# Optimization experiments

Measured on AMD Instinct MI355X. Metric: run time of the kernel, lower is better.

The kernel has to match this reference:

```python
import jax, jax.numpy as jnp
import numpy as np

WS = 8   # window_size
SS = 4   # shift_size
NH = 12  # num_heads
DIM = 384
HD = DIM // NH


def _rel_index():
    coords = np.stack(np.meshgrid(np.arange(WS), np.arange(WS), indexing='ij'))  # (2, ws, ws)
    cf = coords.reshape(2, -1)                       # (2, n)
    rel = (cf[:, :, None] - cf[:, None, :]).transpose(1, 2, 0).copy()  # (n, n, 2)
    rel[..., 0] += WS - 1
    rel[..., 1] += WS - 1
    rel[..., 0] *= 2 * WS - 1
    return rel.sum(-1)                               # (n, n) int


def _attn_mask(h, w):
    img = np.zeros((h, w))
    sl = (slice(0, -WS), slice(-WS, -SS), slice(-SS, None))
    cnt = 0
    for hs in sl:
        for ws_ in sl:
            img[hs, ws_] = cnt
            cnt += 1
    mw = img.reshape(h // WS, WS, w // WS, WS).transpose(0, 2, 1, 3).reshape(-1, WS * WS)  # (nW, n)
    d = mw[:, None, :] - mw[:, :, None]
    return np.where(d != 0, -100.0, 0.0).astype(np.float32)  # (nW, n, n)


def setup_inputs() -> dict:
    key = jax.random.key(0)
    ks = jax.random.split(key, 10)
    B, H, W = 32, 64, 64
    std = 0.02
    return {
        'x': jax.random.normal(ks[0], (B, H, W, DIM), jnp.float32),
        'wq': jax.random.normal(ks[1], (DIM, DIM), jnp.float32) * std,
        'bq': jnp.zeros((DIM,), jnp.float32),
        'wk': jax.random.normal(ks[2], (DIM, DIM), jnp.float32) * std,
        'bk': jnp.zeros((DIM,), jnp.float32),
        'wv': jax.random.normal(ks[3], (DIM, DIM), jnp.float32) * std,
        'bv': jnp.zeros((DIM,), jnp.float32),
        'wo': jax.random.normal(ks[4], (DIM, DIM), jnp.float32) * std,
        'bo': jnp.zeros((DIM,), jnp.float32),
        'bias_table': jax.random.normal(ks[5], ((2 * WS - 1) ** 2, NH), jnp.float32) * std,
    }


def reference(x, wq, bq, wk, bk, wv, bv, wo, bo, bias_table):
    b, h, w, c = x.shape
    pad_h = (-h) % WS
    pad_w = (-w) % WS
    if pad_h or pad_w:
        x = jnp.pad(x, ((0, 0), (0, pad_h), (0, pad_w), (0, 0)))
    hp, wp = x.shape[1], x.shape[2]

    if SS > 0:
        x_sh = jnp.roll(x, shift=(-SS, -SS), axis=(1, 2))
        mask = jnp.asarray(_attn_mask(hp, wp))          # (nW, n, n)
    else:
        x_sh = x
        mask = None

    # window partition -> (B*nW, n, C)
    nwh, nww = hp // WS, wp // WS
    win = x_sh.reshape(b, nwh, WS, nww, WS, c).transpose(0, 1, 3, 2, 4, 5)
    win = win.reshape(-1, WS * WS, c)
    b_, n, _ = win.shape

    scale = HD ** -0.5
    q = (win @ wq.T + bq).reshape(b_, n, NH, HD).transpose(0, 2, 1, 3) * scale
    k = (win @ wk.T + bk).reshape(b_, n, NH, HD).transpose(0, 2, 1, 3)
    v = (win @ wv.T + bv).reshape(b_, n, NH, HD).transpose(0, 2, 1, 3)

    attn = jnp.einsum('bhnd,bhmd->bhnm', q, k)          # (b_, NH, n, n)
    rel = bias_table[jnp.asarray(_rel_index()).reshape(-1)].reshape(n, n, NH)
    attn = attn + rel.transpose(2, 0, 1)[None]
    if mask is not None:
        nW = mask.shape[0]
        attn = attn.reshape(b_ // nW, nW, NH, n, n) + mask[None, :, None]
        attn = attn.reshape(b_, NH, n, n)
    attn = jax.nn.softmax(attn, axis=-1)

    out = jnp.einsum('bhnm,bhmd->bhnd', attn, v).transpose(0, 2, 1, 3).reshape(b_, n, c)
    out = out @ wo.T + bo

    # window reverse -> (B, hp, wp, C)
    out = out.reshape(b, nwh, nww, WS, WS, c).transpose(0, 1, 3, 2, 4, 5).reshape(b, hp, wp, c)
    if SS > 0:
        out = jnp.roll(out, shift=(SS, SS), axis=(1, 2))
    return out[:, :h, :w, :]
```

## Files before the change

### kernel.cpp

```cpp
#include <hip/hip_runtime.h>
#include <hip/hip_bf16.h>

typedef short bf16x8 __attribute__((ext_vector_type(8)));
typedef float f32x4 __attribute__((ext_vector_type(4)));

#define NH_ 12
#define DIM_ 384

static __device__ __forceinline__ float bf2f_us(ushort u) {
    __hip_bfloat16 h; __builtin_memcpy(&h, &u, 2);
    return __bfloat162float(h);
}
static __device__ __forceinline__ ushort f2us(float f) {
    __hip_bfloat16 h = __float2bfloat16(f);
    ushort u; __builtin_memcpy(&u, &h, 2);
    return u;
}

static __device__ __forceinline__ void gload_lds16(const void* g, void* l) {
    __builtin_amdgcn_global_load_lds(
        (const __attribute__((address_space(1))) unsigned int*)g,
        (__attribute__((address_space(3))) unsigned int*)l, 16, 0, 0);
}

static __device__ __forceinline__ int regioncnt(int t, int wr, int wc) {
    int rr = (wr == 7) ? (((t >> 3) < 4) ? 1 : 2) : 0;
    int cc = (wc == 7) ? (((t & 7) < 4) ? 1 : 2) : 0;
    return rr * 3 + cc;
}

__global__ __launch_bounds__(256) void convert_kernel(
    const float* wq, const float* wk, const float* wv, const float* wo,
    const float* bq, const float* bk, const float* bv, const float* bo,
    const float* bt, ushort* __restrict__ dst)
{
    const int N = 594060;
    for (int i = blockIdx.x * 256 + threadIdx.x; i < N; i += gridDim.x * 256) {
        const float* src; int off;
        if (i < 589824) {
            int wsel = i / 147456; off = i - wsel * 147456;
            src = (wsel == 0) ? wq : (wsel == 1) ? wk : (wsel == 2) ? wv : wo;
        } else if (i < 591360) {
            int bsel = (i - 589824) / 384; off = (i - 589824) - bsel * 384;
            src = (bsel == 0) ? bq : (bsel == 1) ? bk : (bsel == 2) ? bv : bo;
        } else {
            off = i - 591360; src = bt;
        }
        dst[i] = f2us(src[off]);
    }
}

__global__ void bias_kernel(const ushort* __restrict__ tablec, float* __restrict__ biasmat) {
    int i = blockIdx.x;
    int j = threadIdx.x;
    int idx = ((i >> 3) - (j >> 3) + 7) * 15 + ((i & 7) - (j & 7) + 7);
    #pragma unroll
    for (int h = 0; h < NH_; ++h)
        biasmat[h * 4096 + i * 64 + j] = bf2f_us(tablec[idx * NH_ + h]);
}

__global__ __launch_bounds__(256, 4) void qkv_gemm(
    const float* __restrict__ x, const ushort* __restrict__ wb,
    ushort* __restrict__ qws, ushort* __restrict__ kws, ushort* __restrict__ vws,
    int wbase, int nmb)
{
    __shared__ __align__(16) ushort As[2][4096];
    __shared__ __align__(16) ushort Bs[2][4096];
    const int nwg = nmb * 9;
    const int orig = blockIdx.x;
    const int wgid = (orig & 7) * (nwg >> 3) + (orig >> 3);
    const int mb = wgid / 9, nt = wgid - mb * 9;
    const int wsel = nt / 3, ntm = nt - wsel * 3;
    const int n0 = nt * 128;
    const int tid = threadIdx.x, lane = tid & 63, wv = tid >> 6;
    const int col16 = lane & 15, quad = lane >> 4;
    const int wm = wv >> 1, wn = wv & 1;

    const int kof = ((tid >> 1) & 3) * 8 + (tid & 1) * 4;
    const float* arow[4];
    #pragma unroll
    for (int it = 0; it < 4; ++it) {
        const int s = it * 128 + (tid >> 1);
        const int row = (s >> 6) * 16 + ((s & 63) >> 2);
        const int wglob = wbase + mb * 2 + (row >> 6);
        const int token = row & 63;
        const int b = wglob >> 6, widx = wglob & 63, wr = widx >> 3, wc = widx & 7;
        const int orr = (wr * 8 + (token >> 3) + 4) & 63;
        const int occ = (wc * 8 + (token & 7) + 4) & 63;
        arow[it] = x + (((size_t)b * 64 + orr) * 64 + occ) * DIM_ + kof;
    }

    const ushort* bsrc = wb + (size_t)n0 * DIM_;
    const int brow_l = lane >> 2, bkof = (lane & 3) * 8;

    f32x4 acc[4][4];
    #pragma unroll
    for (int i2 = 0; i2 < 4; ++i2)
        #pragma unroll
        for (int j2 = 0; j2 < 4; ++j2)
            acc[i2][j2] = (f32x4){0.f, 0.f, 0.f, 0.f};

    const int NK = DIM_ / 32;

    #pragma unroll
    for (int c2 = 0; c2 < 2; ++c2) {
        const int blk = wv * 2 + c2;
        gload_lds16(bsrc + (size_t)(blk * 16 + brow_l) * DIM_ + bkof, &Bs[0][blk * 512]);
    }
    #pragma unroll
    for (int it = 0; it < 4; ++it) {
        const float4 v = *reinterpret_cast<const float4*>(arow[it]);
        ushort4 u4; u4.x = f2us(v.x); u4.y = f2us(v.y); u4.z = f2us(v.z); u4.w = f2us(v.w);
        *reinterpret_cast<ushort4*>(&As[0][it * 1024 + tid * 4]) = u4;
    }
    __syncthreads();

    for (int t = 0; t < NK; ++t) {
        const int cur = t & 1, nxt = cur ^ 1;
        const int kk = t * 32;
        float4 av[4];
        if (t + 1 < NK) {
            #pragma unroll
            for (int it = 0; it < 4; ++it)
                av[it] = *reinterpret_cast<const float4*>(arow[it] + kk + 32);
            #pragma unroll
            for (int c2 = 0; c2 < 2; ++c2) {
                const int blk = wv * 2 + c2;
                gload_lds16(bsrc + (size_t)(blk * 16 + brow_l) * DIM_ + kk + 32 + bkof,
                            &Bs[nxt][blk * 512]);
            }
        }
        bf16x8 af[4], bfm[4];
        #pragma unroll
        for (int rt = 0; rt < 4; ++rt)
            af[rt] = *reinterpret_cast<const bf16x8*>(
                &As[cur][(wm * 4 + rt) * 512 + (col16 * 4 + quad) * 8]);
        #pragma unroll
        for (int ct = 0; ct < 4; ++ct)
            bfm[ct] = *reinterpret_cast<const bf16x8*>(
                &Bs[cur][(wn * 4 + ct) * 512 + (col16 * 4 + quad) * 8]);
        #pragma unroll
        for (int rt = 0; rt < 4; ++rt)
            #pragma unroll
            for (int ct = 0; ct < 4; ++ct)
                acc[rt][ct] = __builtin_amdgcn_mfma_f32_16x16x32_bf16(af[rt], bfm[ct], acc[rt][ct], 0, 0, 0);
        if (t + 1 < NK) {
            #pragma unroll
            for (int it = 0; it < 4; ++it) {
                ushort4 u4;
                u4.x = f2us(av[it].x); u4.y = f2us(av[it].y);
                u4.z = f2us(av[it].z); u4.w = f2us(av[it].w);
                *reinterpret_cast<ushort4*>(&As[nxt][it * 1024 + tid * 4]) = u4;
            }
        }
        __syncthreads();
    }

    const int lw = mb * 2 + wm;
    const float scale = 0.17677669529663687f;
    const ushort* bias_all = wb + 589824 + wsel * 384;
    #pragma unroll
    for (int ct = 0; ct < 4; ++ct) {
        const int jl = ntm * 128 + wn * 64 + ct * 16 + col16;
        const int head = jl >> 5, hd = jl & 31;
        const float bj = bf2f_us(bias_all[jl]);
        #pragma unroll
        for (int rt = 0; rt < 4; ++rt) {
            if (wsel == 2) {
                ushort4 pk;
                pk.x = f2us(acc[rt][ct][0] + bj);
                pk.y = f2us(acc[rt][ct][1] + bj);
                pk.z = f2us(acc[rt][ct][2] + bj);
                pk.w = f2us(acc[rt][ct][3] + bj);
                *reinterpret_cast<ushort4*>(
                    vws + ((size_t)(lw * NH_ + head) * 32 + hd) * 64 + rt * 16 + quad * 4) = pk;
            } else {
                #pragma unroll
                for (int r = 0; r < 4; ++r) {
                    const int token = rt * 16 + quad * 4 + r;
                    const float v = acc[rt][ct][r] + bj;
                    if (wsel == 0)
                        qws[((size_t)(lw * NH_ + head) * 64 + token) * 32 + hd] = f2us(v * scale);
                    else
                        kws[((size_t)(lw * NH_ + head) * 64 + token) * 32 + hd] = f2us(v);
                }
            }
        }
    }
}

__global__ __launch_bounds__(64) void attn_kernel(
    const __hip_bfloat16* __restrict__ qws, const __hip_bfloat16* __restrict__ kws,
    const __hip_bfloat16* __restrict__ vws, const float* __restrict__ biasmat,
    __hip_bfloat16* __restrict__ attnout, int wbase)
{
    __shared__ __align__(16) __hip_bfloat16 Pbuf[64 * 72];
    const int bid = blockIdx.x;
    const int lw = bid / NH_, h = bid - lw * NH_;
    const int w = wbase + lw;
    const int lane = threadIdx.x, col16 = lane & 15, quad = lane >> 4;
    const ushort* qp = reinterpret_cast<const ushort*>(qws) + ((size_t)lw * NH_ + h) * 64 * 32;
    const ushort* kp = reinterpret_cast<const ushort*>(kws) + ((size_t)lw * NH_ + h) * 64 * 32;
    const ushort* vp = reinterpret_cast<const ushort*>(vws) + ((size_t)lw * NH_ + h) * 32 * 64;

    bf16x8 aq[4], bk4[4];
    #pragma unroll
    for (int t = 0; t < 4; ++t) {
        aq[t]  = *reinterpret_cast<const bf16x8*>(qp + (t * 16 + col16) * 32 + quad * 8);
        bk4[t] = *reinterpret_cast<const bf16x8*>(kp + (t * 16 + col16) * 32 + quad * 8);
    }
    f32x4 S[4][4];
    #pragma unroll
    for (int rt = 0; rt < 4; ++rt) {
        #pragma unroll
        for (int ct = 0; ct < 4; ++ct) {
            f32x4 z = {0.f,0.f,0.f,0.f};
            S[rt][ct] = __builtin_amdgcn_mfma_f32_16x16x32_bf16(aq[rt], bk4[ct], z, 0, 0, 0);
        }
    }

    const int widx = w & 63, wr = widx >> 3, wc = widx & 7;
    #pragma unroll
    for (int ct = 0; ct < 4; ++ct) {
        const int jj = ct * 16 + col16;
        const int cntj = regioncnt(jj, wr, wc);
        #pragma unroll
        for (int rt = 0; rt < 4; ++rt) {
            #pragma unroll
            for (int r = 0; r < 4; ++r) {
                const int ii = rt * 16 + quad * 4 + r;
                float add = biasmat[h * 4096 + ii * 64 + jj];
                if (regioncnt(ii, wr, wc) != cntj) add -= 100.f;
                S[rt][ct][r] += add;
            }
        }
    }

    #pragma unroll
    for (int rt = 0; rt < 4; ++rt) {
        float rm[4], rs[4];
        #pragma unroll
        for (int r = 0; r < 4; ++r)
            rm[r] = fmaxf(fmaxf(S[rt][0][r], S[rt][1][r]), fmaxf(S[rt][2][r], S[rt][3][r]));
        #pragma unroll
        for (int d = 1; d <= 8; d <<= 1) {
            #pragma unroll
            for (int r = 0; r < 4; ++r) rm[r] = fmaxf(rm[r], __shfl_xor(rm[r], d, 64));
        }
        #pragma unroll
        for (int r = 0; r < 4; ++r) rs[r] = 0.f;
        #pragma unroll
        for (int ct = 0; ct < 4; ++ct) {
            #pragma unroll
            for (int r = 0; r < 4; ++r) {
                float p = __expf(S[rt][ct][r] - rm[r]);
                S[rt][ct][r] = p;
                rs[r] += p;
            }
        }
        #pragma unroll
        for (int d = 1; d <= 8; d <<= 1) {
            #pragma unroll
            for (int r = 0; r < 4; ++r) rs[r] += __shfl_xor(rs[r], d, 64);
        }
        #pragma unroll
        for (int ct = 0; ct < 4; ++ct) {
            #pragma unroll
            for (int r = 0; r < 4; ++r) {
                const float inv = 1.0f / rs[r];
                Pbuf[(rt * 16 + quad * 4 + r) * 72 + ct * 16 + col16] =
                    __float2bfloat16(S[rt][ct][r] * inv);
            }
        }
    }
    __syncthreads();

    f32x4 O[4][2];
    #pragma unroll
    for (int rt = 0; rt < 4; ++rt) {
        f32x4 z = {0.f,0.f,0.f,0.f};
        O[rt][0] = z; O[rt][1] = z;
    }
    const ushort* pb = reinterpret_cast<const ushort*>(Pbuf);
    #pragma unroll
    for (int ks = 0; ks < 2; ++ks) {
        bf16x8 bv0 = *reinterpret_cast<const bf16x8*>(vp + (col16)*64 + ks * 32 + quad * 8);
        bf16x8 bv1 = *reinterpret_cast<const bf16x8*>(vp + (16 + col16) * 64 + ks * 32 + quad * 8);
        #pragma unroll
        for (int rt = 0; rt < 4; ++rt) {
            bf16x8 ap = *reinterpret_cast<const bf16x8*>(pb + (rt * 16 + col16) * 72 + ks * 32 + quad * 8);
            O[rt][0] = __builtin_amdgcn_mfma_f32_16x16x32_bf16(ap, bv0, O[rt][0], 0, 0, 0);
            O[rt][1] = __builtin_amdgcn_mfma_f32_16x16x32_bf16(ap, bv1, O[rt][1], 0, 0, 0);
        }
    }
    __hip_bfloat16* op = attnout + (size_t)lw * 64 * DIM_ + h * 32;
    #pragma unroll
    for (int rt = 0; rt < 4; ++rt) {
        #pragma unroll
        for (int c2 = 0; c2 < 2; ++c2) {
            #pragma unroll
            for (int r = 0; r < 4; ++r) {
                const int token = rt * 16 + quad * 4 + r;
                op[token * DIM_ + c2 * 16 + col16] = __float2bfloat16(O[rt][c2][r]);
            }
        }
    }
}

__global__ __launch_bounds__(256, 4) void proj_gemm(
    const ushort* __restrict__ attnin, const ushort* __restrict__ wb,
    float* __restrict__ out, int wbase, int nmb)
{
    __shared__ __align__(16) ushort As[2][4096];
    __shared__ __align__(16) ushort Bs[2][4096];
    const int nwg = nmb * 3;
    const int orig = blockIdx.x;
    const int wgid = (orig & 7) * (nwg >> 3) + (orig >> 3);
    const int mb = wgid / 3, nt = wgid - mb * 3;
    const int n0 = nt * 128;
    const int tid = threadIdx.x, lane = tid & 63, wv = tid >> 6;
    const int col16 = lane & 15, quad = lane >> 4;
    const int wm = wv >> 1, wn = wv & 1;

    const ushort* asrc = attnin + (size_t)mb * 128 * DIM_;
    const ushort* bsrc = wb + (size_t)3 * 147456 + (size_t)n0 * DIM_;
    const int row_l = lane >> 2, kof_l = (lane & 3) * 8;

    f32x4 acc[4][4];
    #pragma unroll
    for (int i2 = 0; i2 < 4; ++i2)
        #pragma unroll
        for (int j2 = 0; j2 < 4; ++j2)
            acc[i2][j2] = (f32x4){0.f, 0.f, 0.f, 0.f};

    const int NK = DIM_ / 32;

    #pragma unroll
    for (int c2 = 0; c2 < 2; ++c2) {
        const int blk = wv * 2 + c2;
        gload_lds16(asrc + (size_t)(blk * 16 + row_l) * DIM_ + kof_l, &As[0][blk * 512]);
        gload_lds16(bsrc + (size_t)(blk * 16 + row_l) * DIM_ + kof_l, &Bs[0][blk * 512]);
    }
    __syncthreads();

    for (int t = 0; t < NK; ++t) {
        const int cur = t & 1, nxt = cur ^ 1;
        const int kk = t * 32;
        if (t + 1 < NK) {
            #pragma unroll
            for (int c2 = 0; c2 < 2; ++c2) {
                const int blk = wv * 2 + c2;
                gload_lds16(asrc + (size_t)(blk * 16 + row_l) * DIM_ + kk + 32 + kof_l,
                            &As[nxt][blk * 512]);
                gload_lds16(bsrc + (size_t)(blk * 16 + row_l) * DIM_ + kk + 32 + kof_l,
                            &Bs[nxt][blk * 512]);
            }
        }
        bf16x8 af[4], bfm[4];
        #pragma unroll
        for (int rt = 0; rt < 4; ++rt)
            af[rt] = *reinterpret_cast<const bf16x8*>(
                &As[cur][(wm * 4 + rt) * 512 + (col16 * 4 + quad) * 8]);
        #pragma unroll
        for (int ct = 0; ct < 4; ++ct)
            bfm[ct] = *reinterpret_cast<const bf16x8*>(
                &Bs[cur][(wn * 4 + ct) * 512 + (col16 * 4 + quad) * 8]);
        #pragma unroll
        for (int rt = 0; rt < 4; ++rt)
            #pragma unroll
            for (int ct = 0; ct < 4; ++ct)
                acc[rt][ct] = __builtin_amdgcn_mfma_f32_16x16x32_bf16(af[rt], bfm[ct], acc[rt][ct], 0, 0, 0);
        __syncthreads();
    }

    const int lw = mb * 2 + wm;
    const int wglob = wbase + lw;
    const int b = wglob >> 6, widx = wglob & 63, wr = widx >> 3, wc = widx & 7;
    const ushort* boc = wb + 589824 + 3 * 384;
    #pragma unroll
    for (int ct = 0; ct < 4; ++ct) {
        const int j = n0 + wn * 64 + ct * 16 + col16;
        const float bj = bf2f_us(boc[j]);
        #pragma unroll
        for (int rt = 0; rt < 4; ++rt) {
            #pragma unroll
            for (int r = 0; r < 4; ++r) {
                const int token = rt * 16 + quad * 4 + r;
                const int orr = (wr * 8 + (token >> 3) + 4) & 63;
                const int occ = (wc * 8 + (token & 7) + 4) & 63;
                out[(((size_t)b * 64 + orr) * 64 + occ) * DIM_ + j] = acc[rt][ct][r] + bj;
            }
        }
    }
}

extern "C" void kernel_launch(void* const* d_in, const int* in_sizes, int n_in,
                              void* d_out, int out_size, void* d_ws, size_t ws_size,
                              hipStream_t stream) {
    const float* x = (const float*)d_in[0];
    float* out = (float*)d_out;
    char* ws = (char*)d_ws;

    ushort* wb      = (ushort*)ws;
    float*  biasmat = (float*)(ws + 1188352);
    const size_t FIXED = 1384960;

    int wchunk = 128;
    const int cands[4] = {2048, 1024, 512, 256};
    for (int i = 0; i < 4; ++i) {
        if (FIXED + (size_t)cands[i] * 4 * 49152 <= ws_size) { wchunk = cands[i]; break; }
    }
    const size_t CQ = (size_t)wchunk * NH_ * 64 * 32 * 2;
    __hip_bfloat16* qws = (__hip_bfloat16*)(ws + FIXED);
    __hip_bfloat16* kws = (__hip_bfloat16*)(ws + FIXED + CQ);
    __hip_bfloat16* vws = (__hip_bfloat16*)(ws + FIXED + 2 * CQ);
    __hip_bfloat16* att = (__hip_bfloat16*)(ws + FIXED + 3 * CQ);

    convert_kernel<<<dim3(512), dim3(256), 0, stream>>>(
        (const float*)d_in[1], (const float*)d_in[3], (const float*)d_in[5], (const float*)d_in[7],
        (const float*)d_in[2], (const float*)d_in[4], (const float*)d_in[6], (const float*)d_in[8],
        (const float*)d_in[9], wb);
    bias_kernel<<<dim3(64), dim3(64), 0, stream>>>(wb + 591360, biasmat);

    for (int c = 0; c < 2048 / wchunk; ++c) {
        const int wbase = c * wchunk;
        const int nmb = wchunk / 2;
        qkv_gemm<<<dim3(nmb * 9), dim3(256), 0, stream>>>(
            x, wb, (ushort*)qws, (ushort*)kws, (ushort*)vws, wbase, nmb);
        attn_kernel<<<dim3(wchunk * NH_), dim3(64), 0, stream>>>(qws, kws, vws, biasmat, att, wbase);
        proj_gemm<<<dim3(nmb * 3), dim3(256), 0, stream>>>(
            (const ushort*)att, wb, out, wbase, nmb);
    }
}
```

Measured before the change: 777.6 us.

## Precompute bias+mask in fragment layout, pack 4 heads per attention block, change LDS layout

The bias kernel now builds four window-type variants (interior, last row, last column, corner) of relative-position bias plus shift mask, stored in the MFMA accumulator fragment order, so the attention kernel does coalesced float4 loads instead of scattered scalar loads and per-element region tests. The attention kernel runs four heads per 256-thread block, each wave with its own P buffer, which removes the block-wide barrier. The GEMM kernels also change the LDS tile layout so each lane reads a contiguous 16-byte chunk at lane*8, which aims to cut bank conflicts. The cost is a larger precomputed bias buffer and more LDS per attention block.

```diff
diff --git a/kernel.cpp b/kernel.cpp
--- a/kernel.cpp
+++ b/kernel.cpp
@@ -50,13 +50,32 @@
     }
 }
 
-__global__ void bias_kernel(const ushort* __restrict__ tablec, float* __restrict__ biasmat) {
-    int i = blockIdx.x;
-    int j = threadIdx.x;
-    int idx = ((i >> 3) - (j >> 3) + 7) * 15 + ((i & 7) - (j & 7) + 7);
-    #pragma unroll
-    for (int h = 0; h < NH_; ++h)
-        biasmat[h * 4096 + i * 64 + j] = bf2f_us(tablec[idx * NH_ + h]);
+__global__ __launch_bounds__(256) void bias_kernel(
+    const ushort* __restrict__ tablec, float* __restrict__ biasv)
+{
+    const int vh = blockIdx.x;
+    const int v = vh / NH_, h = vh - v * NH_;
+    const int wr = (v & 2) ? 7 : 0, wc = (v & 1) ? 7 : 0;
+    const int tid = threadIdx.x, lane = tid & 63;
+    #pragma unroll
+    for (int i = 0; i < 4; ++i) {
+        const int tno = (tid >> 6) + 4 * i;
+        const int rt = tno >> 2, ct = tno & 3;
+        const int jj = ct * 16 + (lane & 15);
+        const int cntj = regioncnt(jj, wr, wc);
+        float4 o;
+        float vals[4];
+        #pragma unroll
+        for (int r = 0; r < 4; ++r) {
+            const int ii = rt * 16 + (lane >> 4) * 4 + r;
+            const int idx = ((ii >> 3) - (jj >> 3) + 7) * 15 + ((ii & 7) - (jj & 7) + 7);
+            float val = bf2f_us(tablec[idx * NH_ + h]);
+            if (regioncnt(ii, wr, wc) != cntj) val -= 100.f;
+            vals[r] = val;
+        }
+        o.x = vals[0]; o.y = vals[1]; o.z = vals[2]; o.w = vals[3];
+        reinterpret_cast<float4*>(biasv)[((size_t)vh * 16 + tno) * 64 + lane] = o;
+    }
 }
 
 __global__ __launch_bounds__(256, 4) void qkv_gemm(
@@ -76,22 +95,21 @@
     const int col16 = lane & 15, quad = lane >> 4;
     const int wm = wv >> 1, wn = wv & 1;
 
-    const int kof = ((tid >> 1) & 3) * 8 + (tid & 1) * 4;
+    const int kofA = ((tid >> 5) & 3) * 8 + (tid & 1) * 4;
     const float* arow[4];
     #pragma unroll
     for (int it = 0; it < 4; ++it) {
-        const int s = it * 128 + (tid >> 1);
-        const int row = (s >> 6) * 16 + ((s & 63) >> 2);
+        const int row = (it * 2 + (tid >> 7)) * 16 + ((tid >> 1) & 15);
         const int wglob = wbase + mb * 2 + (row >> 6);
         const int token = row & 63;
         const int b = wglob >> 6, widx = wglob & 63, wr = widx >> 3, wc = widx & 7;
         const int orr = (wr * 8 + (token >> 3) + 4) & 63;
         const int occ = (wc * 8 + (token & 7) + 4) & 63;
-        arow[it] = x + (((size_t)b * 64 + orr) * 64 + occ) * DIM_ + kof;
+        arow[it] = x + (((size_t)b * 64 + orr) * 64 + occ) * DIM_ + kofA;
     }
 
     const ushort* bsrc = wb + (size_t)n0 * DIM_;
-    const int brow_l = lane >> 2, bkof = (lane & 3) * 8;
+    const int brow_l = lane & 15, bkof = (lane >> 4) * 8;
 
     f32x4 acc[4][4];
     #pragma unroll
@@ -133,12 +151,10 @@
         bf16x8 af[4], bfm[4];
         #pragma unroll
         for (int rt = 0; rt < 4; ++rt)
-            af[rt] = *reinterpret_cast<const bf16x8*>(
-                &As[cur][(wm * 4 + rt) * 512 + (col16 * 4 + quad) * 8]);
+            af[rt] = *reinterpret_cast<const bf16x8*>(&As[cur][(wm * 4 + rt) * 512 + lane * 8]);
         #pragma unroll
         for (int ct = 0; ct < 4; ++ct)
-            bfm[ct] = *reinterpret_cast<const bf16x8*>(
-                &Bs[cur][(wn * 4 + ct) * 512 + (col16 * 4 + quad) * 8]);
+            bfm[ct] = *reinterpret_cast<const bf16x8*>(&Bs[cur][(wn * 4 + ct) * 512 + lane * 8]);
         #pragma unroll
         for (int rt = 0; rt < 4; ++rt)
             #pragma unroll
@@ -189,16 +205,18 @@
     }
 }
 
-__global__ __launch_bounds__(64) void attn_kernel(
+__global__ __launch_bounds__(256) void attn_kernel(
     const __hip_bfloat16* __restrict__ qws, const __hip_bfloat16* __restrict__ kws,
-    const __hip_bfloat16* __restrict__ vws, const float* __restrict__ biasmat,
+    const __hip_bfloat16* __restrict__ vws, const float* __restrict__ biasv,
     __hip_bfloat16* __restrict__ attnout, int wbase)
 {
-    __shared__ __align__(16) __hip_bfloat16 Pbuf[64 * 72];
+    __shared__ __align__(16) ushort Pbuf[4][64 * 72];
     const int bid = blockIdx.x;
-    const int lw = bid / NH_, h = bid - lw * NH_;
+    const int lw = bid / 3, hg = bid - lw * 3;
+    const int tid = threadIdx.x, wvi = tid >> 6, lane = tid & 63;
+    const int h = hg * 4 + wvi;
     const int w = wbase + lw;
-    const int lane = threadIdx.x, col16 = lane & 15, quad = lane >> 4;
+    const int col16 = lane & 15, quad = lane >> 4;
     const ushort* qp = reinterpret_cast<const ushort*>(qws) + ((size_t)lw * NH_ + h) * 64 * 32;
     const ushort* kp = reinterpret_cast<const ushort*>(kws) + ((size_t)lw * NH_ + h) * 64 * 32;
     const ushort* vp = reinterpret_cast<const ushort*>(vws) + ((size_t)lw * NH_ + h) * 32 * 64;
@@ -220,22 +238,20 @@
     }
 
     const int widx = w & 63, wr = widx >> 3, wc = widx & 7;
-    #pragma unroll
-    for (int ct = 0; ct < 4; ++ct) {
-        const int jj = ct * 16 + col16;
-        const int cntj = regioncnt(jj, wr, wc);
-        #pragma unroll
-        for (int rt = 0; rt < 4; ++rt) {
-            #pragma unroll
-            for (int r = 0; r < 4; ++r) {
-                const int ii = rt * 16 + quad * 4 + r;
-                float add = biasmat[h * 4096 + ii * 64 + jj];
-                if (regioncnt(ii, wr, wc) != cntj) add -= 100.f;
-                S[rt][ct][r] += add;
-            }
-        }
-    }
-
+    const int v = ((wr == 7) ? 2 : 0) + ((wc == 7) ? 1 : 0);
+    const float4* bp = reinterpret_cast<const float4*>(biasv) +
+                       ((size_t)(v * NH_ + h) * 16) * 64 + lane;
+    #pragma unroll
+    for (int rt = 0; rt < 4; ++rt) {
+        #pragma unroll
+        for (int ct = 0; ct < 4; ++ct) {
+            const float4 bb = bp[(rt * 4 + ct) * 64];
+            S[rt][ct][0] += bb.x; S[rt][ct][1] += bb.y;
+            S[rt][ct][2] += bb.z; S[rt][ct][3] += bb.w;
+        }
+    }
+
+    ushort* pb_w = &Pbuf[wvi][0];
     #pragma unroll
     for (int rt = 0; rt < 4; ++rt) {
         float rm[4], rs[4];
@@ -268,12 +284,11 @@
             #pragma unroll
             for (int r = 0; r < 4; ++r) {
                 const float inv = 1.0f / rs[r];
-                Pbuf[(rt * 16 + quad * 4 + r) * 72 + ct * 16 + col16] =
-                    __float2bfloat16(S[rt][ct][r] * inv);
-            }
-        }
-    }
-    __syncthreads();
+                pb_w[(rt * 16 + quad * 4 + r) * 72 + ct * 16 + col16] =
+                    f2us(S[rt][ct][r] * inv);
+            }
+        }
+    }
 
     f32x4 O[4][2];
     #pragma unroll
@@ -281,14 +296,13 @@
         f32x4 z = {0.f,0.f,0.f,0.f};
         O[rt][0] = z; O[rt][1] = z;
     }
-    const ushort* pb = reinterpret_cast<const ushort*>(Pbuf);
     #pragma unroll
     for (int ks = 0; ks < 2; ++ks) {
         bf16x8 bv0 = *reinterpret_cast<const bf16x8*>(vp + (col16)*64 + ks * 32 + quad * 8);
         bf16x8 bv1 = *reinterpret_cast<const bf16x8*>(vp + (16 + col16) * 64 + ks * 32 + quad * 8);
         #pragma unroll
         for (int rt = 0; rt < 4; ++rt) {
-            bf16x8 ap = *reinterpret_cast<const bf16x8*>(pb + (rt * 16 + col16) * 72 + ks * 32 + quad * 8);
+            bf16x8 ap = *reinterpret_cast<const bf16x8*>(pb_w + (rt * 16 + col16) * 72 + ks * 32 + quad * 8);
             O[rt][0] = __builtin_amdgcn_mfma_f32_16x16x32_bf16(ap, bv0, O[rt][0], 0, 0, 0);
             O[rt][1] = __builtin_amdgcn_mfma_f32_16x16x32_bf16(ap, bv1, O[rt][1], 0, 0, 0);
         }
@@ -324,7 +338,7 @@
 
     const ushort* asrc = attnin + (size_t)mb * 128 * DIM_;
     const ushort* bsrc = wb + (size_t)3 * 147456 + (size_t)n0 * DIM_;
-    const int row_l = lane >> 2, kof_l = (lane & 3) * 8;
+    const int row_l = lane & 15, kof_l = (lane >> 4) * 8;
 
     f32x4 acc[4][4];
     #pragma unroll
@@ -359,12 +373,10 @@
         bf16x8 af[4], bfm[4];
         #pragma unroll
         for (int rt = 0; rt < 4; ++rt)
-            af[rt] = *reinterpret_cast<const bf16x8*>(
-                &As[cur][(wm * 4 + rt) * 512 + (col16 * 4 + quad) * 8]);
+            af[rt] = *reinterpret_cast<const bf16x8*>(&As[cur][(wm * 4 + rt) * 512 + lane * 8]);
         #pragma unroll
         for (int ct = 0; ct < 4; ++ct)
-            bfm[ct] = *reinterpret_cast<const bf16x8*>(
-                &Bs[cur][(wn * 4 + ct) * 512 + (col16 * 4 + quad) * 8]);
+            bfm[ct] = *reinterpret_cast<const bf16x8*>(&Bs[cur][(wn * 4 + ct) * 512 + lane * 8]);
         #pragma unroll
         for (int rt = 0; rt < 4; ++rt)
             #pragma unroll
@@ -401,9 +413,9 @@
     float* out = (float*)d_out;
     char* ws = (char*)d_ws;
 
-    ushort* wb      = (ushort*)ws;
-    float*  biasmat = (float*)(ws + 1188352);
-    const size_t FIXED = 1384960;
+    ushort* wb    = (ushort*)ws;
+    float*  biasv = (float*)(ws + 1188352);
+    const size_t FIXED = 1974784;
 
     int wchunk = 128;
     const int cands[4] = {2048, 1024, 512, 256};
@@ -420,14 +432,15 @@
         (const float*)d_in[1], (const float*)d_in[3], (const float*)d_in[5], (const float*)d_in[7],
         (const float*)d_in[2], (const float*)d_in[4], (const float*)d_in[6], (const float*)d_in[8],
         (const float*)d_in[9], wb);
-    bias_kernel<<<dim3(64), dim3(64), 0, stream>>>(wb + 591360, biasmat);
+    bias_kernel<<<dim3(48), dim3(256), 0, stream>>>(wb + 591360, biasv);
 
     for (int c = 0; c < 2048 / wchunk; ++c) {
         const int wbase = c * wchunk;
         const int nmb = wchunk / 2;
         qkv_gemm<<<dim3(nmb * 9), dim3(256), 0, stream>>>(
             x, wb, (ushort*)qws, (ushort*)kws, (ushort*)vws, wbase, nmb);
-        attn_kernel<<<dim3(wchunk * NH_), dim3(64), 0, stream>>>(qws, kws, vws, biasmat, att, wbase);
+        attn_kernel<<<dim3(wchunk * 3), dim3(256), 0, stream>>>(
+            qws, kws, vws, biasv, att, wbase);
         proj_gemm<<<dim3(nmb * 3), dim3(256), 0, stream>>>(
             (const ushort*)att, wb, out, wbase, nmb);
     }
```

Result: slower. 867.5 us (+11.6%).
